# Kernel optimization log

Measured on AMD Instinct MI355X. Metric: run time of the kernel, lower is better.

The kernel has to match this reference:

```python
import jax, jax.numpy as jnp
import numpy as np

EPS = 1e-5

def _layer_norm(x, w, b):
    m = jnp.mean(x, axis=-1, keepdims=True)
    v = jnp.var(x, axis=-1, keepdims=True)
    return (x - m) * jax.lax.rsqrt(v + EPS) * w + b


def setup_inputs() -> dict:
    key = jax.random.key(0)
    ks = jax.random.split(key, 8)
    N, L, c_s, c_z, H, d = 2, 512, 384, 128, 12, 32
    w_scale = 0.05  # keep logits in a numerically sane range
    return {
        "s": jax.random.normal(ks[0], (N, L, c_s), jnp.float32),
        "z": jax.random.normal(ks[1], (N, L, L, c_z), jnp.float32),
        "ln_s_w": jnp.ones((c_s,), jnp.float32),
        "ln_s_b": jnp.zeros((c_s,), jnp.float32),
        "ln_z_w": jnp.ones((c_z,), jnp.float32),
        "ln_z_b": jnp.zeros((c_z,), jnp.float32),
        "wz": jax.random.normal(ks[2], (H, c_z), jnp.float32) * w_scale,
        "wq": jax.random.normal(ks[3], (c_s, H, d), jnp.float32) * w_scale,
        "wk": jax.random.normal(ks[4], (c_s, H, d), jnp.float32) * w_scale,
        "wv": jax.random.normal(ks[5], (c_s, H, d), jnp.float32) * w_scale,
        "wg": jax.random.normal(ks[6], (c_s, H, d), jnp.float32) * w_scale,
        "bg": jnp.ones((H, d), jnp.float32),
        "wo": jax.random.normal(ks[7], (H, d, c_s), jnp.float32) * w_scale,
        "bo": jnp.zeros((c_s,), jnp.float32),
    }


def reference(s, z, ln_s_w, ln_s_b, ln_z_w, ln_z_b, wz, wq, wk, wv, wg, bg, wo, bo):
    d = wq.shape[-1]
    s_n = _layer_norm(s, ln_s_w, ln_s_b)            # [N,L,c_s]
    z_n = _layer_norm(z, ln_z_w, ln_z_b)            # [N,L,L,c_z]
    bias = jnp.einsum('nijc,hc->nhij', z_n, wz)     # [N,H,L,L] per-head pair bias
    q = jnp.einsum('nlc,chd->nhld', s_n, wq) * (1.0 / jnp.sqrt(jnp.asarray(d, s.dtype)))
    k = jnp.einsum('nlc,chd->nhld', s_n, wk)
    v = jnp.einsum('nlc,chd->nhld', s_n, wv)
    logits = jnp.einsum('nhid,nhjd->nhij', q, k) + bias
    attn = jax.nn.softmax(logits, axis=-1)
    o = jnp.einsum('nhij,nhjd->nihd', attn, v)      # [N,L,H,d]
    g = jax.nn.sigmoid(jnp.einsum('nlc,chd->nlhd', s_n, wg) + bg)
    o = o * g
    out = jnp.einsum('nlhd,hdc->nlc', o, wo) + bo   # [N,L,c_s]
    return out
```

## Files before the change

### kernel.cpp

```cpp
#include <hip/hip_runtime.h>
#include <math.h>

#define N_  2
#define L_  512
#define CS  384
#define CZ  128
#define H_  12
#define D_  32
#define HD  384

__device__ __forceinline__ float sigmoidf_(float x) { return 1.f / (1.f + __expf(-x)); }

__global__ __launch_bounds__(64) void k_ln_s(const float* __restrict__ s,
        const float* __restrict__ w, const float* __restrict__ b,
        float* __restrict__ sn) {
    int row = blockIdx.x;
    const float* x = s + (size_t)row * CS;
    float* y = sn + (size_t)row * CS;
    int lane = threadIdx.x;
    float v[6];
    float sum = 0.f, sq = 0.f;
#pragma unroll
    for (int e = 0; e < 6; ++e) {
        v[e] = x[lane + e * 64];
        sum += v[e];
        sq  += v[e] * v[e];
    }
#pragma unroll
    for (int o = 1; o < 64; o <<= 1) {
        sum += __shfl_xor(sum, o);
        sq  += __shfl_xor(sq , o);
    }
    float m = sum * (1.f / CS);
    float var = sq * (1.f / CS) - m * m;
    float rstd = rsqrtf(var + 1e-5f);
#pragma unroll
    for (int e = 0; e < 6; ++e) {
        int c = lane + e * 64;
        y[c] = (v[e] - m) * rstd * w[c] + b[c];
    }
}

__global__ __launch_bounds__(128) void k_wz_prep(const float* __restrict__ lnzw,
        const float* __restrict__ lnzb, const float* __restrict__ wz,
        float* __restrict__ wzp, float* __restrict__ wzps, float* __restrict__ wzb) {
    __shared__ float sp[H_][CZ];
    __shared__ float sb[H_][CZ];
    int c = threadIdx.x;
    float lw = lnzw[c], lb = lnzb[c];
    for (int h = 0; h < H_; ++h) {
        float w = wz[h * CZ + c];
        float p = lw * w;
        sp[h][c] = p;
        sb[h][c] = lb * w;
        wzp[h * CZ + c] = p;
    }
    __syncthreads();
    if (c < H_) {
        float s1 = 0.f, s2 = 0.f;
        for (int e = 0; e < CZ; ++e) { s1 += sp[c][e]; s2 += sb[c][e]; }
        wzps[c] = s1; wzb[c] = s2;
    }
}

__global__ __launch_bounds__(384) void k_proj(const float* __restrict__ sn,
        const float* __restrict__ wq, const float* __restrict__ wk,
        const float* __restrict__ wv, const float* __restrict__ wg,
        float* __restrict__ q, float* __restrict__ k, float* __restrict__ v,
        float* __restrict__ g) {
    __shared__ float s_lds[8][CS];
    int t = threadIdx.x;
    int row0 = blockIdx.x * 8;
    {
        const float4* src = (const float4*)(sn + (size_t)row0 * CS);
        float4* dst = (float4*)(&s_lds[0][0]);
        dst[t] = src[t];
        dst[t + 384] = src[t + 384];
    }
    __syncthreads();
    int mat = t / 96;
    int col = (t % 96) * 4;
    const float* W = (mat == 0) ? wq : (mat == 1) ? wk : (mat == 2) ? wv : wg;
    float acc[8][4];
#pragma unroll
    for (int r = 0; r < 8; ++r)
#pragma unroll
        for (int j = 0; j < 4; ++j) acc[r][j] = 0.f;
    for (int kk = 0; kk < CS; kk += 4) {
        float4 w0 = *(const float4*)(W + (size_t)(kk + 0) * HD + col);
        float4 w1 = *(const float4*)(W + (size_t)(kk + 1) * HD + col);
        float4 w2 = *(const float4*)(W + (size_t)(kk + 2) * HD + col);
        float4 w3 = *(const float4*)(W + (size_t)(kk + 3) * HD + col);
#pragma unroll
        for (int r = 0; r < 8; ++r) {
            float4 sv = *(const float4*)(&s_lds[r][kk]);
            acc[r][0] += sv.x * w0.x + sv.y * w1.x + sv.z * w2.x + sv.w * w3.x;
            acc[r][1] += sv.x * w0.y + sv.y * w1.y + sv.z * w2.y + sv.w * w3.y;
            acc[r][2] += sv.x * w0.z + sv.y * w1.z + sv.z * w2.z + sv.w * w3.z;
            acc[r][3] += sv.x * w0.w + sv.y * w1.w + sv.z * w2.w + sv.w * w3.w;
        }
    }
    float* out = (mat == 0) ? q : (mat == 1) ? k : (mat == 2) ? v : g;
    float scale = (mat == 0) ? 0.17677669529663687f : 1.f;
#pragma unroll
    for (int r = 0; r < 8; ++r) {
        float4 o;
        o.x = acc[r][0] * scale; o.y = acc[r][1] * scale;
        o.z = acc[r][2] * scale; o.w = acc[r][3] * scale;
        *(float4*)(out + (size_t)(row0 + r) * HD + col) = o;
    }
}

__global__ __launch_bounds__(384) void k_bias(const float* __restrict__ z,
        const float* __restrict__ wzp, const float* __restrict__ wzps,
        const float* __restrict__ wzb, float* __restrict__ bias) {
    __shared__ float z_lds[32][132];
    __shared__ float w_lds[H_][132];
    __shared__ float m_lds[32], r_lds[32];
    __shared__ float ws_lds[H_], wb_lds[H_];
    int t = threadIdx.x;
    int jt = blockIdx.x, i = blockIdx.y, n = blockIdx.z;
    int j0 = jt * 32;
    {
        int h = t >> 5, c4 = t & 31;
        *(float4*)(&w_lds[h][c4 * 4]) = *(const float4*)(wzp + h * CZ + c4 * 4);
        if (t < H_) { ws_lds[t] = wzps[t]; wb_lds[t] = wzb[t]; }
    }
    {
        const float4* src = (const float4*)(z + ((size_t)(n * L_ + i) * L_ + j0) * CZ);
        int idx = t;
        *(float4*)(&z_lds[idx >> 5][(idx & 31) * 4]) = src[idx];
        idx = t + 384;
        *(float4*)(&z_lds[idx >> 5][(idx & 31) * 4]) = src[idx];
        if (t < 256) {
            idx = t + 768;
            *(float4*)(&z_lds[idx >> 5][(idx & 31) * 4]) = src[idx];
        }
    }
    __syncthreads();
    if (t < 256) {
        int r = t >> 3, lane = t & 7;
        float s1 = 0.f, s2 = 0.f;
#pragma unroll
        for (int e4 = 0; e4 < 4; ++e4) {
            float4 v = *(const float4*)(&z_lds[r][lane * 16 + e4 * 4]);
            s1 += v.x + v.y + v.z + v.w;
            s2 += v.x * v.x + v.y * v.y + v.z * v.z + v.w * v.w;
        }
#pragma unroll
        for (int o = 1; o < 8; o <<= 1) { s1 += __shfl_xor(s1, o); s2 += __shfl_xor(s2, o); }
        if (lane == 0) {
            float m = s1 * (1.f / CZ);
            float var = s2 * (1.f / CZ) - m * m;
            m_lds[r] = m;
            r_lds[r] = rsqrtf(var + 1e-5f);
        }
    }
    __syncthreads();
    int hg = t >> 7;
    int j  = (t >> 2) & 31;
    int cs = t & 3;
    const float* zr = &z_lds[j][cs * 32];
    const float* wr0 = &w_lds[hg * 4 + 0][cs * 32];
    const float* wr1 = &w_lds[hg * 4 + 1][cs * 32];
    const float* wr2 = &w_lds[hg * 4 + 2][cs * 32];
    const float* wr3 = &w_lds[hg * 4 + 3][cs * 32];
    float a0 = 0.f, a1 = 0.f, a2 = 0.f, a3 = 0.f;
#pragma unroll
    for (int e = 0; e < 8; ++e) {
        float4 zv = *(const float4*)(zr + e * 4);
        float4 w0 = *(const float4*)(wr0 + e * 4);
        float4 w1 = *(const float4*)(wr1 + e * 4);
        float4 w2 = *(const float4*)(wr2 + e * 4);
        float4 w3 = *(const float4*)(wr3 + e * 4);
        a0 += zv.x * w0.x + zv.y * w0.y + zv.z * w0.z + zv.w * w0.w;
        a1 += zv.x * w1.x + zv.y * w1.y + zv.z * w1.z + zv.w * w1.w;
        a2 += zv.x * w2.x + zv.y * w2.y + zv.z * w2.z + zv.w * w2.w;
        a3 += zv.x * w3.x + zv.y * w3.y + zv.z * w3.z + zv.w * w3.w;
    }
    a0 += __shfl_xor(a0, 1); a0 += __shfl_xor(a0, 2);
    a1 += __shfl_xor(a1, 1); a1 += __shfl_xor(a1, 2);
    a2 += __shfl_xor(a2, 1); a2 += __shfl_xor(a2, 2);
    a3 += __shfl_xor(a3, 1); a3 += __shfl_xor(a3, 2);
    float dot = (cs == 0) ? a0 : (cs == 1) ? a1 : (cs == 2) ? a2 : a3;
    int hh = hg * 4 + cs;
    float bv = r_lds[j] * (dot - m_lds[j] * ws_lds[hh]) + wb_lds[hh];
    bias[(((size_t)n * H_ + hh) * L_ + i) * L_ + j0 + j] = bv;
}

__global__ __launch_bounds__(512) void k_attn(const float* __restrict__ q,
        const float* __restrict__ k, const float* __restrict__ v,
        const float* __restrict__ gpre, const float* __restrict__ bg,
        const float* __restrict__ bias, float* __restrict__ og) {
    __shared__ float t_lds[2][64][36];
    int t = threadIdx.x;
    int lane = t & 63;
    int w = t >> 6;
    int it = blockIdx.x, h = blockIdx.y, n = blockIdx.z;
    int i = it * 8 + w;
    int srow = t >> 3, se = t & 7;

    const float* qrow = q + ((size_t)(n * L_) + i) * HD + h * D_;
    float4 qr[8];
#pragma unroll
    for (int d4 = 0; d4 < 8; ++d4) qr[d4] = *(const float4*)(qrow + d4 * 4);
    const float* brow = bias + (((size_t)n * H_ + h) * L_ + i) * L_;
    const float* kbase = k + (size_t)(n * L_) * HD + h * D_;
    const float* vbase = v + (size_t)(n * L_) * HD + h * D_;

    *(float4*)(&t_lds[0][srow][se * 4]) =
        *(const float4*)(kbase + (size_t)srow * HD + se * 4);
    __syncthreads();
    float p[8];
#pragma unroll
    for (int s = 0; s < 8; ++s) {
        float4 stg;
        if (s < 7)
            stg = *(const float4*)(kbase + (size_t)((s + 1) * 64 + srow) * HD + se * 4);
        float acc = brow[s * 64 + lane];
        const float* kr = &t_lds[s & 1][lane][0];
#pragma unroll
        for (int d4 = 0; d4 < 8; ++d4) {
            float4 kv = *(const float4*)(kr + d4 * 4);
            float4 qv = qr[d4];
            acc += qv.x * kv.x + qv.y * kv.y + qv.z * kv.z + qv.w * kv.w;
        }
        p[s] = acc;
        if (s < 7)
            *(float4*)(&t_lds[(s + 1) & 1][srow][se * 4]) = stg;
        __syncthreads();
    }
    float mx = p[0];
#pragma unroll
    for (int s = 1; s < 8; ++s) mx = fmaxf(mx, p[s]);
#pragma unroll
    for (int o = 1; o < 64; o <<= 1) mx = fmaxf(mx, __shfl_xor(mx, o));
    float sum = 0.f;
#pragma unroll
    for (int s = 0; s < 8; ++s) { p[s] = __expf(p[s] - mx); sum += p[s]; }
#pragma unroll
    for (int o = 1; o < 64; o <<= 1) sum += __shfl_xor(sum, o);
    float rinv = 1.f / sum;

    float acc[32];
#pragma unroll
    for (int d = 0; d < 32; ++d) acc[d] = 0.f;
    *(float4*)(&t_lds[0][srow][se * 4]) =
        *(const float4*)(vbase + (size_t)srow * HD + se * 4);
    __syncthreads();
#pragma unroll
    for (int s = 0; s < 8; ++s) {
        float4 stg;
        if (s < 7)
            stg = *(const float4*)(vbase + (size_t)((s + 1) * 64 + srow) * HD + se * 4);
        float e = p[s];
        const float* vr = &t_lds[s & 1][lane][0];
#pragma unroll
        for (int d4 = 0; d4 < 8; ++d4) {
            float4 vv = *(const float4*)(vr + d4 * 4);
            acc[d4 * 4 + 0] += e * vv.x;
            acc[d4 * 4 + 1] += e * vv.y;
            acc[d4 * 4 + 2] += e * vv.z;
            acc[d4 * 4 + 3] += e * vv.w;
        }
        if (s < 7)
            *(float4*)(&t_lds[(s + 1) & 1][srow][se * 4]) = stg;
        __syncthreads();
    }
    bool b0 = lane & 1, b1 = lane & 2, b2 = lane & 4, b3 = lane & 8, b4 = lane & 16;
    float r1[16];
#pragma unroll
    for (int m = 0; m < 16; ++m) {
        float give = b0 ? acc[2 * m] : acc[2 * m + 1];
        float got = __shfl_xor(give, 1);
        r1[m] = (b0 ? acc[2 * m + 1] : acc[2 * m]) + got;
    }
    float r2[8];
#pragma unroll
    for (int m = 0; m < 8; ++m) {
        float give = b1 ? r1[2 * m] : r1[2 * m + 1];
        float got = __shfl_xor(give, 2);
        r2[m] = (b1 ? r1[2 * m + 1] : r1[2 * m]) + got;
    }
    float r3[4];
#pragma unroll
    for (int m = 0; m < 4; ++m) {
        float give = b2 ? r2[2 * m] : r2[2 * m + 1];
        float got = __shfl_xor(give, 4);
        r3[m] = (b2 ? r2[2 * m + 1] : r2[2 * m]) + got;
    }
    float r4[2];
#pragma unroll
    for (int m = 0; m < 2; ++m) {
        float give = b3 ? r3[2 * m] : r3[2 * m + 1];
        float got = __shfl_xor(give, 8);
        r4[m] = (b3 ? r3[2 * m + 1] : r3[2 * m]) + got;
    }
    float give = b4 ? r4[0] : r4[1];
    float r5 = (b4 ? r4[1] : r4[0]) + __shfl_xor(give, 16);
    float oval = (r5 + __shfl_xor(r5, 32)) * rinv;

    if (lane < 32) {
        int d = lane;
        size_t gi = ((size_t)(n * L_) + i) * HD + h * D_ + d;
        float g = sigmoidf_(gpre[gi] + bg[h * D_ + d]);
        og[gi] = oval * g;
    }
}

__global__ __launch_bounds__(384) void k_out(const float* __restrict__ og,
        const float* __restrict__ wo, const float* __restrict__ bo,
        float* __restrict__ out) {
    __shared__ float o_lds[8][HD];
    int t = threadIdx.x;
    int row0 = blockIdx.x * 8;
    {
        const float4* src = (const float4*)(og + (size_t)row0 * HD);
        float4* dst = (float4*)(&o_lds[0][0]);
        dst[t] = src[t];
        dst[t + 384] = src[t + 384];
    }
    __syncthreads();
    float acc[8];
#pragma unroll
    for (int r = 0; r < 8; ++r) acc[r] = 0.f;
    for (int kk = 0; kk < HD; kk += 4) {
        float w0 = wo[(size_t)(kk + 0) * CS + t];
        float w1 = wo[(size_t)(kk + 1) * CS + t];
        float w2 = wo[(size_t)(kk + 2) * CS + t];
        float w3 = wo[(size_t)(kk + 3) * CS + t];
#pragma unroll
        for (int r = 0; r < 8; ++r) {
            float4 ov = *(const float4*)(&o_lds[r][kk]);
            acc[r] += ov.x * w0 + ov.y * w1 + ov.z * w2 + ov.w * w3;
        }
    }
    float bv = bo[t];
#pragma unroll
    for (int r = 0; r < 8; ++r) out[(size_t)(row0 + r) * CS + t] = acc[r] + bv;
}

extern "C" void kernel_launch(void* const* d_in, const int* in_sizes, int n_in,
                              void* d_out, int out_size, void* d_ws, size_t ws_size,
                              hipStream_t stream) {
    const float* s    = (const float*)d_in[0];
    const float* z    = (const float*)d_in[1];
    const float* lnsw = (const float*)d_in[2];
    const float* lnsb = (const float*)d_in[3];
    const float* lnzw = (const float*)d_in[4];
    const float* lnzb = (const float*)d_in[5];
    const float* wz   = (const float*)d_in[6];
    const float* wq   = (const float*)d_in[7];
    const float* wk   = (const float*)d_in[8];
    const float* wv   = (const float*)d_in[9];
    const float* wg   = (const float*)d_in[10];
    const float* bg   = (const float*)d_in[11];
    const float* wo   = (const float*)d_in[12];
    const float* bo   = (const float*)d_in[13];
    float* out = (float*)d_out;

    float* ws = (float*)d_ws;
    const size_t NL = (size_t)N_ * L_;
    float* sn   = ws;  ws += NL * CS;
    float* q    = ws;  ws += NL * HD;
    float* kk   = ws;  ws += NL * HD;
    float* vv   = ws;  ws += NL * HD;
    float* gpre = ws;  ws += NL * HD;
    float* og   = ws;  ws += NL * HD;
    float* wzp  = ws;  ws += H_ * CZ;
    float* wzps = ws;  ws += 16;
    float* wzb  = ws;  ws += 16;
    float* bias = ws;

    k_ln_s<<<dim3(NL), 64, 0, stream>>>(s, lnsw, lnsb, sn);
    k_wz_prep<<<dim3(1), 128, 0, stream>>>(lnzw, lnzb, wz, wzp, wzps, wzb);
    k_proj<<<dim3(128), 384, 0, stream>>>(sn, wq, wk, wv, wg, q, kk, vv, gpre);
    k_bias<<<dim3(16, 512, 2), 384, 0, stream>>>(z, wzp, wzps, wzb, bias);
    k_attn<<<dim3(64, 12, 2), 512, 0, stream>>>(q, kk, vv, gpre, bg, bias, og);
    k_out<<<dim3(128), 384, 0, stream>>>(og, wo, bo, out);
}
```

Before: 543.6 us.

## Retile pair-bias kernel to 128 columns with per-thread 2-row, 12-head register tiles

The pair-bias kernel now stages 128 z rows per block instead of 32 and uses 256 threads. Each thread accumulates dot products for two rows across all 12 heads in registers. The LayerNorm mean and variance are computed in the same pass over LDS, which removes a separate statistics phase and one barrier. Results are written as float2 pairs. The goal is more reuse of the weight and z values per LDS read and fewer small blocks. In exchange, the block needs roughly 70KB of LDS, which limits how many blocks fit on a CU and may reduce latency hiding for this bandwidth-heavy kernel.

```diff
diff --git a/kernel.cpp b/kernel.cpp
--- a/kernel.cpp
+++ b/kernel.cpp
@@ -111,81 +111,85 @@
     }
 }
 
-__global__ __launch_bounds__(384) void k_bias(const float* __restrict__ z,
+__global__ __launch_bounds__(256) void k_bias(const float* __restrict__ z,
         const float* __restrict__ wzp, const float* __restrict__ wzps,
         const float* __restrict__ wzb, float* __restrict__ bias) {
-    __shared__ float z_lds[32][132];
-    __shared__ float w_lds[H_][132];
-    __shared__ float m_lds[32], r_lds[32];
+    __shared__ float z_lds[128 * 130];
+    __shared__ float w_lds[H_ * CZ];
     __shared__ float ws_lds[H_], wb_lds[H_];
     int t = threadIdx.x;
     int jt = blockIdx.x, i = blockIdx.y, n = blockIdx.z;
-    int j0 = jt * 32;
+    int j0 = jt * 128;
     {
-        int h = t >> 5, c4 = t & 31;
-        *(float4*)(&w_lds[h][c4 * 4]) = *(const float4*)(wzp + h * CZ + c4 * 4);
-        if (t < H_) { ws_lds[t] = wzps[t]; wb_lds[t] = wzb[t]; }
+        const float4* wsrc = (const float4*)wzp;
+        float4* wdst = (float4*)w_lds;
+        if (t < 128) {
+            wdst[t] = wsrc[t];
+            wdst[t + 128] = wsrc[t + 128];
+            wdst[t + 256] = wsrc[t + 256];
+        } else if (t < 128 + H_) {
+            ws_lds[t - 128] = wzps[t - 128];
+            wb_lds[t - 128] = wzb[t - 128];
+        }
     }
     {
         const float4* src = (const float4*)(z + ((size_t)(n * L_ + i) * L_ + j0) * CZ);
-        int idx = t;
-        *(float4*)(&z_lds[idx >> 5][(idx & 31) * 4]) = src[idx];
-        idx = t + 384;
-        *(float4*)(&z_lds[idx >> 5][(idx & 31) * 4]) = src[idx];
-        if (t < 256) {
-            idx = t + 768;
-            *(float4*)(&z_lds[idx >> 5][(idx & 31) * 4]) = src[idx];
-        }
-    }
-    __syncthreads();
-    if (t < 256) {
-        int r = t >> 3, lane = t & 7;
-        float s1 = 0.f, s2 = 0.f;
-#pragma unroll
-        for (int e4 = 0; e4 < 4; ++e4) {
-            float4 v = *(const float4*)(&z_lds[r][lane * 16 + e4 * 4]);
-            s1 += v.x + v.y + v.z + v.w;
-            s2 += v.x * v.x + v.y * v.y + v.z * v.z + v.w * v.w;
-        }
-#pragma unroll
-        for (int o = 1; o < 8; o <<= 1) { s1 += __shfl_xor(s1, o); s2 += __shfl_xor(s2, o); }
-        if (lane == 0) {
-            float m = s1 * (1.f / CZ);
-            float var = s2 * (1.f / CZ) - m * m;
-            m_lds[r] = m;
-            r_lds[r] = rsqrtf(var + 1e-5f);
-        }
-    }
-    __syncthreads();
-    int hg = t >> 7;
-    int j  = (t >> 2) & 31;
-    int cs = t & 3;
-    const float* zr = &z_lds[j][cs * 32];
-    const float* wr0 = &w_lds[hg * 4 + 0][cs * 32];
-    const float* wr1 = &w_lds[hg * 4 + 1][cs * 32];
-    const float* wr2 = &w_lds[hg * 4 + 2][cs * 32];
-    const float* wr3 = &w_lds[hg * 4 + 3][cs * 32];
-    float a0 = 0.f, a1 = 0.f, a2 = 0.f, a3 = 0.f;
-#pragma unroll
-    for (int e = 0; e < 8; ++e) {
-        float4 zv = *(const float4*)(zr + e * 4);
-        float4 w0 = *(const float4*)(wr0 + e * 4);
-        float4 w1 = *(const float4*)(wr1 + e * 4);
-        float4 w2 = *(const float4*)(wr2 + e * 4);
-        float4 w3 = *(const float4*)(wr3 + e * 4);
-        a0 += zv.x * w0.x + zv.y * w0.y + zv.z * w0.z + zv.w * w0.w;
-        a1 += zv.x * w1.x + zv.y * w1.y + zv.z * w1.z + zv.w * w1.w;
-        a2 += zv.x * w2.x + zv.y * w2.y + zv.z * w2.z + zv.w * w2.w;
-        a3 += zv.x * w3.x + zv.y * w3.y + zv.z * w3.z + zv.w * w3.w;
-    }
-    a0 += __shfl_xor(a0, 1); a0 += __shfl_xor(a0, 2);
-    a1 += __shfl_xor(a1, 1); a1 += __shfl_xor(a1, 2);
-    a2 += __shfl_xor(a2, 1); a2 += __shfl_xor(a2, 2);
-    a3 += __shfl_xor(a3, 1); a3 += __shfl_xor(a3, 2);
-    float dot = (cs == 0) ? a0 : (cs == 1) ? a1 : (cs == 2) ? a2 : a3;
-    int hh = hg * 4 + cs;
-    float bv = r_lds[j] * (dot - m_lds[j] * ws_lds[hh]) + wb_lds[hh];
-    bias[(((size_t)n * H_ + hh) * L_ + i) * L_ + j0 + j] = bv;
+#pragma unroll
+        for (int e = 0; e < 16; ++e) {
+            int idx = t + e * 256;
+            float4 vv = src[idx];
+            *(float4*)(&z_lds[(idx >> 5) * 130 + (idx & 31) * 4]) = vv;
+        }
+    }
+    __syncthreads();
+    int l = t & 63, w = t >> 6;
+    int jj = (l & 7) | ((l >> 5) << 3);
+    int cs = (l >> 3) & 3;
+    int r0 = w * 32 + jj * 2;
+    const float* zr0 = &z_lds[r0 * 130];
+    const float* zr1 = zr0 + 130;
+    float acc0[H_], acc1[H_];
+#pragma unroll
+    for (int h = 0; h < H_; ++h) { acc0[h] = 0.f; acc1[h] = 0.f; }
+    float s10 = 0.f, s20 = 0.f, s11 = 0.f, s21 = 0.f;
+#pragma unroll
+    for (int k = 0; k < 8; ++k) {
+        int col = cs * 4 + k * 16;
+        float4 z0 = *(const float4*)(zr0 + col);
+        float4 z1 = *(const float4*)(zr1 + col);
+        s10 += z0.x + z0.y + z0.z + z0.w;
+        s20 += z0.x * z0.x + z0.y * z0.y + z0.z * z0.z + z0.w * z0.w;
+        s11 += z1.x + z1.y + z1.z + z1.w;
+        s21 += z1.x * z1.x + z1.y * z1.y + z1.z * z1.z + z1.w * z1.w;
+#pragma unroll
+        for (int h = 0; h < H_; ++h) {
+            float4 wv = *(const float4*)(&w_lds[h * CZ + col]);
+            acc0[h] += z0.x * wv.x + z0.y * wv.y + z0.z * wv.z + z0.w * wv.w;
+            acc1[h] += z1.x * wv.x + z1.y * wv.y + z1.z * wv.z + z1.w * wv.w;
+        }
+    }
+#pragma unroll
+    for (int h = 0; h < H_; ++h) {
+        acc0[h] += __shfl_xor(acc0[h], 8);  acc0[h] += __shfl_xor(acc0[h], 16);
+        acc1[h] += __shfl_xor(acc1[h], 8);  acc1[h] += __shfl_xor(acc1[h], 16);
+    }
+    s10 += __shfl_xor(s10, 8); s10 += __shfl_xor(s10, 16);
+    s20 += __shfl_xor(s20, 8); s20 += __shfl_xor(s20, 16);
+    s11 += __shfl_xor(s11, 8); s11 += __shfl_xor(s11, 16);
+    s21 += __shfl_xor(s21, 8); s21 += __shfl_xor(s21, 16);
+    float m0 = s10 * (1.f / CZ), m1 = s11 * (1.f / CZ);
+    float rs0 = rsqrtf(s20 * (1.f / CZ) - m0 * m0 + 1e-5f);
+    float rs1 = rsqrtf(s21 * (1.f / CZ) - m1 * m1 + 1e-5f);
+    int jg = j0 + r0;
+#pragma unroll
+    for (int hh = 0; hh < 3; ++hh) {
+        int h = hh * 4 + cs;
+        float wsh = ws_lds[h], wbh = wb_lds[h];
+        float2 bv;
+        bv.x = rs0 * (acc0[h] - m0 * wsh) + wbh;
+        bv.y = rs1 * (acc1[h] - m1 * wsh) + wbh;
+        *(float2*)(&bias[(((size_t)n * H_ + h) * L_ + i) * L_ + jg]) = bv;
+    }
 }
 
 __global__ __launch_bounds__(512) void k_attn(const float* __restrict__ q,
@@ -375,7 +379,7 @@
     k_ln_s<<<dim3(NL), 64, 0, stream>>>(s, lnsw, lnsb, sn);
     k_wz_prep<<<dim3(1), 128, 0, stream>>>(lnzw, lnzb, wz, wzp, wzps, wzb);
     k_proj<<<dim3(128), 384, 0, stream>>>(sn, wq, wk, wv, wg, q, kk, vv, gpre);
-    k_bias<<<dim3(16, 512, 2), 384, 0, stream>>>(z, wzp, wzps, wzb, bias);
+    k_bias<<<dim3(4, 512, 2), 256, 0, stream>>>(z, wzp, wzps, wzb, bias);
     k_attn<<<dim3(64, 12, 2), 512, 0, stream>>>(q, kk, vv, gpre, bg, bias, og);
     k_out<<<dim3(128), 384, 0, stream>>>(og, wo, bo, out);
 }
```

Measured after the change: 568.0 us. +4.5%, slower.
